# Kernel tuning notes

Hardware: AMD Instinct MI355X
Metric: run time of the kernel (lower is better)

The kernel has to match this reference:

```python
import jax, jax.numpy as jnp
import numpy as np
import math

B, S, E, H = 2, 4096, 1024, 1024

def setup_inputs() -> dict:
    key = jax.random.key(0)
    ks = jax.random.split(key, 7)
    X = jax.random.normal(ks[0], (B, S, E), dtype=jnp.float32)
    attention_mask = jnp.ones((B, S, S), dtype=jnp.int32)
    sc = 1.0 / math.sqrt(E)
    Wq = jax.random.normal(ks[1], (H, E), dtype=jnp.float32) * sc
    Wk = jax.random.normal(ks[2], (H, E), dtype=jnp.float32) * sc
    Wv = jax.random.normal(ks[3], (H, E), dtype=jnp.float32) * sc
    bq = jnp.zeros((H,), dtype=jnp.float32)
    bk = jnp.zeros((H,), dtype=jnp.float32)
    bv = jnp.zeros((H,), dtype=jnp.float32)
    return {"X": X, "attention_mask": attention_mask,
            "Wq": Wq, "bq": bq, "Wk": Wk, "bk": bk, "Wv": Wv, "bv": bv}

def reference(X, attention_mask, Wq, bq, Wk, bk, Wv, bv):
    # Linear layers: y = x @ W^T + b (torch convention W is [out, in])
    Q = jnp.einsum('bse,he->bsh', X, Wq) + bq
    K = jnp.einsum('bse,he->bsh', X, Wk) + bk
    V = jnp.einsum('bse,he->bsh', X, Wv) + bv
    scale = 1.0 / math.sqrt(H)
    scores = jnp.einsum('bqh,bkh->bqk', Q, K) * scale  # [B,S,S]
    scores = jnp.where(attention_mask == 0, -jnp.inf, scores)
    # dropout (eval mode -> identity) would be applied here, BEFORE softmax
    weights = jax.nn.softmax(scores, axis=-1)
    out = jnp.einsum('bqk,bkh->bqh', weights, V)  # [B,S,H]
    return out
```

## Files before the change

kernel.cpp:

```cpp
#include <hip/hip_runtime.h>
#include <stdint.h>


typedef __bf16 bf16;
typedef __attribute__((ext_vector_type(4))) __bf16 bf16x4;
typedef __attribute__((ext_vector_type(8))) __bf16 bf16x8;
typedef __attribute__((ext_vector_type(4))) float f32x4;

__device__ __forceinline__ void g2l16(const void* g, void* l) {
  __builtin_amdgcn_global_load_lds(
      (const __attribute__((address_space(1))) uint32_t*)g,
      (__attribute__((address_space(3))) uint32_t*)l, 16, 0, 0);
}

template <int V> struct IC { static constexpr int value = V; };

__device__ __forceinline__ void waitvm_rt(int vm) {
  if (vm == 6) asm volatile("s_waitcnt vmcnt(6)" ::: "memory");
  else if (vm == 4) asm volatile("s_waitcnt vmcnt(4)" ::: "memory");
  else if (vm == 0) asm volatile("s_waitcnt vmcnt(0)" ::: "memory");
}

__global__ __launch_bounds__(256) void cvt_f32_bf16(
    const float* __restrict__ src, bf16* __restrict__ dst, int n) {
  const int i = (blockIdx.x * 256 + threadIdx.x) * 8;
  if (i >= n) return;
  f32x4 a = *(const f32x4*)(src + i);
  f32x4 b = *(const f32x4*)(src + i + 4);
  bf16x8 o;
#pragma unroll
  for (int e = 0; e < 4; ++e) { o[e] = (bf16)a[e]; o[4 + e] = (bf16)b[e]; }
  *(bf16x8*)(dst + i) = o;
}

__global__ __launch_bounds__(256) void cvt_w3(
    const float* __restrict__ Wq, const float* __restrict__ Wk,
    const float* __restrict__ Wv, bf16* __restrict__ dst) {
  const int i = (blockIdx.x * 256 + threadIdx.x) * 8;
  const int seg = i >> 20;
  const int off = i & 1048575;
  const float* src = (seg == 0) ? Wq : (seg == 1) ? Wk : Wv;
  f32x4 a = *(const f32x4*)(src + off);
  f32x4 b = *(const f32x4*)(src + off + 4);
  bf16x8 o;
#pragma unroll
  for (int e = 0; e < 4; ++e) { o[e] = (bf16)a[e]; o[4 + e] = (bf16)b[e]; }
  *(bf16x8*)(dst + i) = o;
}

template <int NT>
__device__ __forceinline__ void kloop256(
    const bf16* __restrict__ Ag, const bf16* __restrict__ Bg, const int KA,
    const int KB, bf16* lds, f32x4 (&acc)[8][4]) {
  const int tid = threadIdx.x;
  const int lane = tid & 63, wave = tid >> 6;
  const int l15 = lane & 15, quad = lane >> 4;
  const int wrow = (wave >> 2) * 128;
  const int wcol = (wave & 3) * 64;
  const int srow = tid >> 3;
  const int scol = ((tid & 7) ^ (srow & 7)) * 8;
  const int swz = l15 & 7;

  auto stg = [&](int t, int h) {
    bf16* base = lds + (t & 1) * 32768;
    if (h == 0) {
      const bf16* g = Bg + (size_t)srow * KB + t * 64 + scol;
      g2l16(g, base + 16384 + tid * 8);
      g2l16(g + (size_t)64 * KB, base + 16384 + tid * 8 + 4096);
    } else if (h == 1) {
      const bf16* g = Bg + (size_t)(128 + srow) * KB + t * 64 + scol;
      g2l16(g, base + 24576 + tid * 8);
      g2l16(g + (size_t)64 * KB, base + 24576 + tid * 8 + 4096);
    } else if (h == 2) {
      const bf16* g = Ag + (size_t)srow * KA + t * 64 + scol;
      g2l16(g, base + tid * 8);
      g2l16(g + (size_t)128 * KA, base + tid * 8 + 8192);
    } else {
      const bf16* g = Ag + (size_t)(64 + srow) * KA + t * 64 + scol;
      g2l16(g, base + 4096 + tid * 8);
      g2l16(g + (size_t)128 * KA, base + 4096 + tid * 8 + 8192);
    }
  };

  bf16x8 bq[2][4];
  auto phase = [&](int t, auto qc, int st, int sh, bool ds, int vm) {
    constexpr int q = decltype(qc)::value;
    bf16* base = lds + (t & 1) * 32768;
    bf16x8 af[2][2];
#pragma unroll
    for (int i = 0; i < 2; ++i)
#pragma unroll
      for (int ks = 0; ks < 2; ++ks)
        af[i][ks] = *(const bf16x8*)&base[
            (wrow + (2 * q + i) * 16 + l15) * 64 + ((ks * 4 + quad) ^ swz) * 8];
    if constexpr (q == 0) {
#pragma unroll
      for (int j = 0; j < 4; ++j)
#pragma unroll
        for (int ks = 0; ks < 2; ++ks)
          bq[ks][j] = *(const bf16x8*)&base[16384 +
              (wcol + j * 16 + l15) * 64 + ((ks * 4 + quad) ^ swz) * 8];
    }
    if (ds) stg(st, sh);
    __builtin_amdgcn_s_barrier();
    asm volatile("s_waitcnt lgkmcnt(0)" ::: "memory");
    __builtin_amdgcn_sched_barrier(0);
    __builtin_amdgcn_s_setprio(1);
#pragma unroll
    for (int ks = 0; ks < 2; ++ks)
#pragma unroll
      for (int i = 0; i < 2; ++i)
#pragma unroll
        for (int j = 0; j < 4; ++j)
          acc[2 * q + i][j] = __builtin_amdgcn_mfma_f32_16x16x32_bf16(
              af[i][ks], bq[ks][j], acc[2 * q + i][j], 0, 0, 0);
    __builtin_amdgcn_s_setprio(0);
    waitvm_rt(vm);
    __builtin_amdgcn_s_barrier();
  };

  stg(0, 0); stg(0, 1); stg(0, 2); stg(0, 3);
  stg(1, 0); stg(1, 1); stg(1, 2);
  asm volatile("s_waitcnt vmcnt(6)" ::: "memory");
  __builtin_amdgcn_s_barrier();

  constexpr int NI = NT / 2;
#pragma unroll 1
  for (int u = 0; u < NI; ++u) {
    const int t0 = 2 * u, t1 = t0 + 1;
    const bool nl = (u + 1 < NI);
    phase(t0, IC<0>{}, t1, 3, true, -1);
    phase(t0, IC<1>{}, t0 + 2, 0, nl, -1);
    phase(t0, IC<2>{}, t0 + 2, 1, nl, -1);
    phase(t0, IC<3>{}, t0 + 2, 2, nl, nl ? 6 : 0);
    phase(t1, IC<0>{}, t0 + 2, 3, nl, -1);
    phase(t1, IC<1>{}, t0 + 3, 0, nl, -1);
    phase(t1, IC<2>{}, t0 + 3, 1, nl, -1);
    phase(t1, IC<3>{}, t0 + 3, 2, nl, nl ? 6 : -1);
  }
}

template <int NT>
__device__ __forceinline__ void kloop128(
    const bf16* __restrict__ Ag, const bf16* __restrict__ Bg, const int KA,
    const int KB, bf16* lds, f32x4 (&acc)[4][4]) {
  const int tid = threadIdx.x;
  const int lane = tid & 63, wave = tid >> 6;
  const int l15 = lane & 15, quad = lane >> 4;
  const int wrow = (wave >> 1) * 64;
  const int wcol = (wave & 1) * 64;
  const int srow = tid >> 3;
  const int scol = ((tid & 7) ^ (srow & 7)) * 8;
  const int swz = l15 & 7;
  const int s5 = srow >> 5;
  const int r31 = srow & 31;

  auto stg = [&](int t, int h) {
    bf16* base = lds + (t & 1) * 24576;
    if (h == 0) {
      const bf16* g = Bg + (size_t)srow * KB + t * 64 + scol;
      g2l16(g, base + 16384 + tid * 8);
      g2l16(g + (size_t)64 * KB, base + 16384 + tid * 8 + 4096);
    } else {
      const int r0 = s5 * 64 + ((h == 2) ? 32 : 0) + r31;
      const bf16* g = Ag + (size_t)r0 * KA + t * 64 + scol;
      bf16* d = base + ((h == 2) ? 2048 : 0) + s5 * 4096 + r31 * 64 +
                (tid & 7) * 8;
      g2l16(g, d);
      g2l16(g + (size_t)128 * KA, d + 8192);
    }
  };

  bf16x8 bq[2][4];
  auto phase = [&](int t, auto mhc, int st1, int sh1, int st2, int sh2,
                   bool ds, int vm) {
    constexpr int mh = decltype(mhc)::value;
    bf16* base = lds + (t & 1) * 24576;
    bf16x8 af[2][2];
#pragma unroll
    for (int i = 0; i < 2; ++i)
#pragma unroll
      for (int ks = 0; ks < 2; ++ks)
        af[i][ks] = *(const bf16x8*)&base[
            (wrow + (2 * mh + i) * 16 + l15) * 64 +
            ((ks * 4 + quad) ^ swz) * 8];
    if constexpr (mh == 0) {
#pragma unroll
      for (int j = 0; j < 4; ++j)
#pragma unroll
        for (int ks = 0; ks < 2; ++ks)
          bq[ks][j] = *(const bf16x8*)&base[16384 +
              (wcol + j * 16 + l15) * 64 + ((ks * 4 + quad) ^ swz) * 8];
    }
    if (ds) { stg(st1, sh1); if (sh2 >= 0) stg(st2, sh2); }
    __builtin_amdgcn_s_barrier();
    asm volatile("s_waitcnt lgkmcnt(0)" ::: "memory");
    __builtin_amdgcn_sched_barrier(0);
    __builtin_amdgcn_s_setprio(1);
#pragma unroll
    for (int ks = 0; ks < 2; ++ks)
#pragma unroll
      for (int i = 0; i < 2; ++i)
#pragma unroll
        for (int j = 0; j < 4; ++j)
          acc[2 * mh + i][j] = __builtin_amdgcn_mfma_f32_16x16x32_bf16(
              af[i][ks], bq[ks][j], acc[2 * mh + i][j], 0, 0, 0);
    __builtin_amdgcn_s_setprio(0);
    waitvm_rt(vm);
    __builtin_amdgcn_s_barrier();
  };

  stg(0, 0); stg(0, 1); stg(0, 2);
  stg(1, 0); stg(1, 1);
  asm volatile("s_waitcnt vmcnt(4)" ::: "memory");
  __builtin_amdgcn_s_barrier();

  constexpr int NI = NT / 2;
#pragma unroll 1
  for (int u = 0; u < NI; ++u) {
    const int t0 = 2 * u, t1 = t0 + 1;
    const bool nl = (u + 1 < NI);
    phase(t0, IC<0>{}, t1, 2, -1, -1, true, -1);
    phase(t0, IC<1>{}, t0 + 2, 0, t0 + 2, 1, nl, nl ? 4 : 0);
    phase(t1, IC<0>{}, t0 + 2, 2, -1, -1, nl, -1);
    phase(t1, IC<1>{}, t0 + 3, 0, t0 + 3, 1, nl, nl ? 4 : -1);
  }
}

__global__ __launch_bounds__(512, 2) void gemm_qkv(
    const bf16* __restrict__ Xb, const bf16* __restrict__ Wb3,
    const float* __restrict__ bq, const float* __restrict__ bk,
    const float* __restrict__ bv, bf16* __restrict__ QK,
    bf16* __restrict__ Vt) {
  __shared__ __align__(16) bf16 lds[2 * 24576];
  const int which = blockIdx.y >> 3;
  const int n0 = (blockIdx.y & 7) * 128;
  const int m0 = blockIdx.x * 256;
  const bf16* Ag = Xb + (size_t)m0 * 1024;
  const bf16* Bg = Wb3 + (size_t)which * 1048576 + (size_t)n0 * 1024;
  const float* bias = (which == 0) ? bq : ((which == 1) ? bk : bv);

  f32x4 acc[4][4];
#pragma unroll
  for (int i = 0; i < 4; ++i)
#pragma unroll
    for (int j = 0; j < 4; ++j) acc[i][j] = f32x4{0.f, 0.f, 0.f, 0.f};

  kloop128<16>(Ag, Bg, 1024, 1024, lds, acc);

  const int lane = threadIdx.x & 63, wave = threadIdx.x >> 6;
  const int l15 = lane & 15, quad = lane >> 4;
  const int wrow = (wave >> 1) * 64, wcol = (wave & 1) * 64;

  if (which < 2) {
    bf16* C = QK + (size_t)which * (size_t)(8192 * 1024);
#pragma unroll
    for (int i = 0; i < 4; ++i) {
      const int r = m0 + wrow + i * 16 + quad * 4;
#pragma unroll
      for (int j = 0; j < 4; ++j) {
        const int c = n0 + wcol + j * 16 + l15;
        const float bvv = bias[c];
        f32x4 v = acc[i][j];
#pragma unroll
        for (int reg = 0; reg < 4; ++reg)
          C[(size_t)(r + reg) * 1024 + c] = (bf16)(v[reg] + bvv);
      }
    }
  } else {
#pragma unroll
    for (int i = 0; i < 4; ++i) {
      const int r = m0 + wrow + i * 16 + quad * 4;
      const int b = r >> 12, s = r & 4095;
#pragma unroll
      for (int j = 0; j < 4; ++j) {
        const int c = n0 + wcol + j * 16 + l15;
        const float bvv = bias[c];
        f32x4 v = acc[i][j];
        bf16x4 o;
#pragma unroll
        for (int reg = 0; reg < 4; ++reg) o[reg] = (bf16)(v[reg] + bvv);
        *(bf16x4*)&Vt[((size_t)(b * 1024 + c)) * 4096 + s] = o;
      }
    }
  }
}

__global__ __launch_bounds__(512, 2) void gemm_scores(
    const bf16* __restrict__ Q, const bf16* __restrict__ Kb,
    const int* __restrict__ mask, bf16* __restrict__ P,
    float* __restrict__ row_sum) {
  __shared__ __align__(16) bf16 lds[2 * 32768];
  const int m0 = blockIdx.x * 256;
  const int n0 = blockIdx.y * 256;
  const int batch = m0 >> 12;
  const bf16* Ag = Q + (size_t)m0 * 1024;
  const bf16* Bg = Kb + (size_t)batch * (size_t)(4096 * 1024) +
                   (size_t)n0 * 1024;

  f32x4 acc[8][4];
#pragma unroll
  for (int i = 0; i < 8; ++i)
#pragma unroll
    for (int j = 0; j < 4; ++j) acc[i][j] = f32x4{0.f, 0.f, 0.f, 0.f};

  kloop256<16>(Ag, Bg, 1024, 1024, lds, acc);

  const int lane = threadIdx.x & 63, wave = threadIdx.x >> 6;
  const int l15 = lane & 15, quad = lane >> 4;
  const int wrow = (wave >> 2) * 128, wcol = (wave & 3) * 64;

#pragma unroll
  for (int i = 0; i < 8; ++i) {
    const int r = m0 + wrow + i * 16 + quad * 4;
    f32x4 rsum = f32x4{0.f, 0.f, 0.f, 0.f};
#pragma unroll
    for (int j = 0; j < 4; ++j) {
      const int c = n0 + wcol + j * 16 + l15;
      f32x4 v = acc[i][j];
#pragma unroll
      for (int reg = 0; reg < 4; ++reg) {
        float e = __expf(v[reg] * 0.03125f);
        if (mask[(size_t)(r + reg) * 4096 + c] == 0) e = 0.f;
        P[(size_t)(r + reg) * 4096 + c] = (bf16)e;
        rsum[reg] += e;
      }
    }
#pragma unroll
    for (int off = 1; off < 16; off <<= 1) {
#pragma unroll
      for (int reg = 0; reg < 4; ++reg)
        rsum[reg] += __shfl_xor(rsum[reg], off);
    }
    if (l15 == 0) {
#pragma unroll
      for (int reg = 0; reg < 4; ++reg)
        atomicAdd(&row_sum[r + reg], rsum[reg]);
    }
  }
}

__global__ __launch_bounds__(512, 2) void gemm_pv(
    const bf16* __restrict__ Pm, const bf16* __restrict__ Vt,
    const float* __restrict__ row_sum, float* __restrict__ C) {
  __shared__ __align__(16) bf16 lds[2 * 24576];
  const int m0 = blockIdx.x * 256;
  const int n0 = blockIdx.y * 128;
  const int batch = m0 >> 12;
  const bf16* Ag = Pm + (size_t)m0 * 4096;
  const bf16* Bg = Vt + ((size_t)batch * 1024 + n0) * 4096;

  f32x4 acc[4][4];
#pragma unroll
  for (int i = 0; i < 4; ++i)
#pragma unroll
    for (int j = 0; j < 4; ++j) acc[i][j] = f32x4{0.f, 0.f, 0.f, 0.f};

  kloop128<64>(Ag, Bg, 4096, 4096, lds, acc);

  const int lane = threadIdx.x & 63, wave = threadIdx.x >> 6;
  const int l15 = lane & 15, quad = lane >> 4;
  const int wrow = (wave >> 1) * 64, wcol = (wave & 1) * 64;

#pragma unroll
  for (int i = 0; i < 4; ++i) {
    const int r = m0 + wrow + i * 16 + quad * 4;
    const f32x4 rs = *(const f32x4*)&row_sum[r];
    f32x4 inv;
#pragma unroll
    for (int reg = 0; reg < 4; ++reg) inv[reg] = 1.0f / rs[reg];
#pragma unroll
    for (int j = 0; j < 4; ++j) {
      const int c = n0 + wcol + j * 16 + l15;
      f32x4 v = acc[i][j];
#pragma unroll
      for (int reg = 0; reg < 4; ++reg)
        C[(size_t)(r + reg) * 1024 + c] = v[reg] * inv[reg];
    }
  }
}

extern "C" void kernel_launch(void* const* d_in, const int* in_sizes, int n_in,
                              void* d_out, int out_size, void* d_ws,
                              size_t ws_size, hipStream_t stream) {
  const float* X   = (const float*)d_in[0];
  const int* mask  = (const int*)d_in[1];
  const float* Wq  = (const float*)d_in[2];
  const float* bq  = (const float*)d_in[3];
  const float* Wk  = (const float*)d_in[4];
  const float* bk  = (const float*)d_in[5];
  const float* Wv  = (const float*)d_in[6];
  const float* bv  = (const float*)d_in[7];
  float* out = (float*)d_out;

  const size_t QKV_ELEMS = (size_t)8192 * 1024;
  bf16* Q    = (bf16*)d_ws;
  bf16* Kb   = Q + QKV_ELEMS;
  bf16* X_bf = Kb + QKV_ELEMS;
  bf16* Vt   = X_bf + QKV_ELEMS;
  bf16* Sc   = Vt + QKV_ELEMS;
  bf16* W_bf = Sc;
  float* row_sum = (float*)X_bf;

  cvt_f32_bf16<<<dim3(4096), dim3(256), 0, stream>>>(X, X_bf, 8388608);
  cvt_w3<<<dim3(1536), dim3(256), 0, stream>>>(Wq, Wk, Wv, W_bf);
  gemm_qkv<<<dim3(32, 24), dim3(512), 0, stream>>>(X_bf, W_bf, bq, bk, bv, Q,
                                                   Vt);
  hipMemsetAsync(row_sum, 0, 8192 * sizeof(float), stream);
  gemm_scores<<<dim3(32, 16), dim3(512), 0, stream>>>(Q, Kb, mask, Sc,
                                                      row_sum);
  gemm_pv<<<dim3(32, 8), dim3(512), 0, stream>>>(Sc, Vt, row_sum, out);
}
```

Before: 434.3 us.

## Peel last K-loop iteration, move LDS wait after MFMAs, remap blocks per XCD

The K-loop phases now take compile-time flags, and the final iteration is peeled so the steady-state loop carries no runtime branches for staging or vmcnt waits. The lgkmcnt(0) wait and sched_barrier before the MFMA block are removed and the wait is placed after the MFMAs. This lets LDS fragment reads overlap matrix math, relying on the compiler to insert the needed waits. All three GEMMs also remap block IDs so consecutive blocks on the same XCD (bid&7) cover contiguous tiles, aiming at better L2 reuse. The risk is that the compiler-inserted waits or a changed schedule regress, and the swizzle formulas assume fixed grid sizes.

Measured after the change: 448.9 us. 1.03x slower.

```diff
diff --git a/kernel.cpp b/kernel.cpp
--- a/kernel.cpp
+++ b/kernel.cpp
@@ -14,11 +14,12 @@
 }
 
 template <int V> struct IC { static constexpr int value = V; };
-
-__device__ __forceinline__ void waitvm_rt(int vm) {
-  if (vm == 6) asm volatile("s_waitcnt vmcnt(6)" ::: "memory");
-  else if (vm == 4) asm volatile("s_waitcnt vmcnt(4)" ::: "memory");
-  else if (vm == 0) asm volatile("s_waitcnt vmcnt(0)" ::: "memory");
+template <bool V> struct BC { static constexpr bool value = V; };
+
+template <int N> __device__ __forceinline__ void waitvm() {
+  if constexpr (N == 6) asm volatile("s_waitcnt vmcnt(6)" ::: "memory");
+  else if constexpr (N == 4) asm volatile("s_waitcnt vmcnt(4)" ::: "memory");
+  else if constexpr (N == 0) asm volatile("s_waitcnt vmcnt(0)" ::: "memory");
 }
 
 __global__ __launch_bounds__(256) void cvt_f32_bf16(
@@ -83,8 +84,10 @@
   };
 
   bf16x8 bq[2][4];
-  auto phase = [&](int t, auto qc, int st, int sh, bool ds, int vm) {
+  auto phase = [&](int t, auto qc, int st, int sh, auto dsc, auto vmc) {
     constexpr int q = decltype(qc)::value;
+    constexpr bool ds = decltype(dsc)::value;
+    constexpr int vm = decltype(vmc)::value;
     bf16* base = lds + (t & 1) * 32768;
     bf16x8 af[2][2];
 #pragma unroll
@@ -101,10 +104,8 @@
           bq[ks][j] = *(const bf16x8*)&base[16384 +
               (wcol + j * 16 + l15) * 64 + ((ks * 4 + quad) ^ swz) * 8];
     }
-    if (ds) stg(st, sh);
+    if constexpr (ds) stg(st, sh);
     __builtin_amdgcn_s_barrier();
-    asm volatile("s_waitcnt lgkmcnt(0)" ::: "memory");
-    __builtin_amdgcn_sched_barrier(0);
     __builtin_amdgcn_s_setprio(1);
 #pragma unroll
     for (int ks = 0; ks < 2; ++ks)
@@ -115,7 +116,8 @@
           acc[2 * q + i][j] = __builtin_amdgcn_mfma_f32_16x16x32_bf16(
               af[i][ks], bq[ks][j], acc[2 * q + i][j], 0, 0, 0);
     __builtin_amdgcn_s_setprio(0);
-    waitvm_rt(vm);
+    asm volatile("s_waitcnt lgkmcnt(0)" ::: "memory");
+    waitvm<vm>();
     __builtin_amdgcn_s_barrier();
   };
 
@@ -126,17 +128,27 @@
 
   constexpr int NI = NT / 2;
 #pragma unroll 1
-  for (int u = 0; u < NI; ++u) {
+  for (int u = 0; u < NI - 1; ++u) {
     const int t0 = 2 * u, t1 = t0 + 1;
-    const bool nl = (u + 1 < NI);
-    phase(t0, IC<0>{}, t1, 3, true, -1);
-    phase(t0, IC<1>{}, t0 + 2, 0, nl, -1);
-    phase(t0, IC<2>{}, t0 + 2, 1, nl, -1);
-    phase(t0, IC<3>{}, t0 + 2, 2, nl, nl ? 6 : 0);
-    phase(t1, IC<0>{}, t0 + 2, 3, nl, -1);
-    phase(t1, IC<1>{}, t0 + 3, 0, nl, -1);
-    phase(t1, IC<2>{}, t0 + 3, 1, nl, -1);
-    phase(t1, IC<3>{}, t0 + 3, 2, nl, nl ? 6 : -1);
+    phase(t0, IC<0>{}, t1, 3, BC<true>{}, IC<-1>{});
+    phase(t0, IC<1>{}, t0 + 2, 0, BC<true>{}, IC<-1>{});
+    phase(t0, IC<2>{}, t0 + 2, 1, BC<true>{}, IC<-1>{});
+    phase(t0, IC<3>{}, t0 + 2, 2, BC<true>{}, IC<6>{});
+    phase(t1, IC<0>{}, t0 + 2, 3, BC<true>{}, IC<-1>{});
+    phase(t1, IC<1>{}, t0 + 3, 0, BC<true>{}, IC<-1>{});
+    phase(t1, IC<2>{}, t0 + 3, 1, BC<true>{}, IC<-1>{});
+    phase(t1, IC<3>{}, t0 + 3, 2, BC<true>{}, IC<6>{});
+  }
+  {
+    const int t0 = NT - 2, t1 = NT - 1;
+    phase(t0, IC<0>{}, t1, 3, BC<true>{}, IC<-1>{});
+    phase(t0, IC<1>{}, 0, 0, BC<false>{}, IC<-1>{});
+    phase(t0, IC<2>{}, 0, 0, BC<false>{}, IC<-1>{});
+    phase(t0, IC<3>{}, 0, 0, BC<false>{}, IC<0>{});
+    phase(t1, IC<0>{}, 0, 0, BC<false>{}, IC<-1>{});
+    phase(t1, IC<1>{}, 0, 0, BC<false>{}, IC<-1>{});
+    phase(t1, IC<2>{}, 0, 0, BC<false>{}, IC<-1>{});
+    phase(t1, IC<3>{}, 0, 0, BC<false>{}, IC<-1>{});
   }
 }
 
@@ -172,9 +184,11 @@
   };
 
   bf16x8 bq[2][4];
-  auto phase = [&](int t, auto mhc, int st1, int sh1, int st2, int sh2,
-                   bool ds, int vm) {
+  auto phase = [&](int t, auto mhc, int st1, int sh1, int st2, auto dsc,
+                   auto vmc) {
     constexpr int mh = decltype(mhc)::value;
+    constexpr int ds = decltype(dsc)::value;
+    constexpr int vm = decltype(vmc)::value;
     bf16* base = lds + (t & 1) * 24576;
     bf16x8 af[2][2];
 #pragma unroll
@@ -192,10 +206,9 @@
           bq[ks][j] = *(const bf16x8*)&base[16384 +
               (wcol + j * 16 + l15) * 64 + ((ks * 4 + quad) ^ swz) * 8];
     }
-    if (ds) { stg(st1, sh1); if (sh2 >= 0) stg(st2, sh2); }
+    if constexpr (ds >= 1) stg(st1, sh1);
+    if constexpr (ds == 2) stg(st2, sh1 + 1);
     __builtin_amdgcn_s_barrier();
-    asm volatile("s_waitcnt lgkmcnt(0)" ::: "memory");
-    __builtin_amdgcn_sched_barrier(0);
     __builtin_amdgcn_s_setprio(1);
 #pragma unroll
     for (int ks = 0; ks < 2; ++ks)
@@ -206,7 +219,8 @@
           acc[2 * mh + i][j] = __builtin_amdgcn_mfma_f32_16x16x32_bf16(
               af[i][ks], bq[ks][j], acc[2 * mh + i][j], 0, 0, 0);
     __builtin_amdgcn_s_setprio(0);
-    waitvm_rt(vm);
+    asm volatile("s_waitcnt lgkmcnt(0)" ::: "memory");
+    waitvm<vm>();
     __builtin_amdgcn_s_barrier();
   };
 
@@ -217,13 +231,19 @@
 
   constexpr int NI = NT / 2;
 #pragma unroll 1
-  for (int u = 0; u < NI; ++u) {
+  for (int u = 0; u < NI - 1; ++u) {
     const int t0 = 2 * u, t1 = t0 + 1;
-    const bool nl = (u + 1 < NI);
-    phase(t0, IC<0>{}, t1, 2, -1, -1, true, -1);
-    phase(t0, IC<1>{}, t0 + 2, 0, t0 + 2, 1, nl, nl ? 4 : 0);
-    phase(t1, IC<0>{}, t0 + 2, 2, -1, -1, nl, -1);
-    phase(t1, IC<1>{}, t0 + 3, 0, t0 + 3, 1, nl, nl ? 4 : -1);
+    phase(t0, IC<0>{}, t1, 2, 0, IC<1>{}, IC<-1>{});
+    phase(t0, IC<1>{}, t0 + 2, 0, t0 + 2, IC<2>{}, IC<4>{});
+    phase(t1, IC<0>{}, t0 + 2, 2, 0, IC<1>{}, IC<-1>{});
+    phase(t1, IC<1>{}, t0 + 3, 0, t0 + 3, IC<2>{}, IC<4>{});
+  }
+  {
+    const int t0 = NT - 2, t1 = NT - 1;
+    phase(t0, IC<0>{}, t1, 2, 0, IC<1>{}, IC<-1>{});
+    phase(t0, IC<1>{}, 0, 0, 0, IC<0>{}, IC<0>{});
+    phase(t1, IC<0>{}, 0, 0, 0, IC<0>{}, IC<-1>{});
+    phase(t1, IC<1>{}, 0, 0, 0, IC<0>{}, IC<-1>{});
   }
 }
 
@@ -233,9 +253,12 @@
     const float* __restrict__ bv, bf16* __restrict__ QK,
     bf16* __restrict__ Vt) {
   __shared__ __align__(16) bf16 lds[2 * 24576];
-  const int which = blockIdx.y >> 3;
-  const int n0 = (blockIdx.y & 7) * 128;
-  const int m0 = blockIdx.x * 256;
+  const int bid = blockIdx.y * 32 + blockIdx.x;
+  const int sb = (bid & 7) * 96 + (bid >> 3);
+  const int bx = sb & 31, by = sb >> 5;
+  const int which = by >> 3;
+  const int n0 = (by & 7) * 128;
+  const int m0 = bx * 256;
   const bf16* Ag = Xb + (size_t)m0 * 1024;
   const bf16* Bg = Wb3 + (size_t)which * 1048576 + (size_t)n0 * 1024;
   const float* bias = (which == 0) ? bq : ((which == 1) ? bk : bv);
@@ -291,8 +314,11 @@
     const int* __restrict__ mask, bf16* __restrict__ P,
     float* __restrict__ row_sum) {
   __shared__ __align__(16) bf16 lds[2 * 32768];
-  const int m0 = blockIdx.x * 256;
-  const int n0 = blockIdx.y * 256;
+  const int bid = blockIdx.y * 32 + blockIdx.x;
+  const int sb = (bid & 7) * 64 + (bid >> 3);
+  const int bx = sb & 31, by = sb >> 5;
+  const int m0 = bx * 256;
+  const int n0 = by * 256;
   const int batch = m0 >> 12;
   const bf16* Ag = Q + (size_t)m0 * 1024;
   const bf16* Bg = Kb + (size_t)batch * (size_t)(4096 * 1024) +
@@ -344,8 +370,11 @@
     const bf16* __restrict__ Pm, const bf16* __restrict__ Vt,
     const float* __restrict__ row_sum, float* __restrict__ C) {
   __shared__ __align__(16) bf16 lds[2 * 24576];
-  const int m0 = blockIdx.x * 256;
-  const int n0 = blockIdx.y * 128;
+  const int bid = blockIdx.y * 32 + blockIdx.x;
+  const int sb = (bid & 7) * 32 + (bid >> 3);
+  const int bx = sb & 31, by = sb >> 5;
+  const int m0 = bx * 256;
+  const int n0 = by * 128;
   const int batch = m0 >> 12;
   const bf16* Ag = Pm + (size_t)m0 * 4096;
   const bf16* Bg = Vt + ((size_t)batch * 1024 + n0) * 4096;
```
